# Kernel optimization log

Measured on AMD Instinct MI355X. Metric: run time of the kernel, lower is better.

## Reference

```python
import jax, jax.numpy as jnp
import numpy as np

B = 2_000_000
L = 64
STEPS = 10
LAT_CONST = 5 * 0.03 / 200 + 0.06  # queue*lat/bw + 0.06
GRAD_CONST = 1.0 / 0.06
SEND_CONST = 2.0 / 3.0


def setup_inputs() -> dict:
    key = jax.random.key(0)
    ks = jax.random.split(key, 5)
    x = jax.random.normal(ks[0], (B, 7), dtype=jnp.float32)
    # column 0 is the loop counter i; program assumes it starts at 0 -> 10 iterations
    x = x.at[:, 0].set(0.0)
    W1 = jax.random.normal(ks[1], (3, L), dtype=jnp.float32) * 0.1
    b1 = jnp.zeros((L,), dtype=jnp.float32)
    W2 = jax.random.normal(ks[2], (L, L), dtype=jnp.float32) * 0.1
    b2 = jnp.zeros((L,), dtype=jnp.float32)
    W3 = jax.random.normal(ks[3], (L, 1), dtype=jnp.float32) * 0.1
    b3 = jnp.zeros((1,), dtype=jnp.float32)
    return {"x": x, "W1": W1, "b1": b1, "W2": W2, "b2": b2, "W3": W3, "b3": b3}


def _mlp(feat, W1, b1, W2, b2, W3, b3):
    h = jax.nn.relu(feat @ W1 + b1)
    h = jax.nn.relu(h @ W2 + b2)
    return jax.nn.sigmoid(h @ W3 + b3)[:, 0]


def reference(x, W1, b1, W2, b2, W3, b3):
    def step(state, _):
        x2 = state[:, 2]
        x6 = state[:, 6]
        # IfElse on column 6 vs comparison_bar=0.0:
        #   body  (x6 <= 0): x2 * (x6 + 1)          (assign_upper_sender_ratio)
        #   else  (x6 >  0): x2 * ((1 - x6) / 1)    (assign_down_sender_ratio, sub_l = left-sub)
        x2 = jnp.where(x6 <= 0.0, x2 * (x6 + 1.0), x2 * (1.0 - x6))
        x4 = x2 + LAT_CONST            # latency_ratio
        x5 = x2 * SEND_CONST           # sending_ratio
        x3 = x4 * GRAD_CONST           # latency_gradient
        feat = jnp.stack([x3, x4, x5], axis=1)  # [B,3]
        a = _mlp(feat, W1, b1, W2, b2, W3, b3)  # new action -> column 2
        new_state = state.at[:, 0].add(1.0)
        new_state = new_state.at[:, 2].set(a)
        new_state = new_state.at[:, 3].set(x3)
        new_state = new_state.at[:, 4].set(x4)
        new_state = new_state.at[:, 5].set(x5)
        return new_state, None

    final, _ = jax.lax.scan(step, x, None, length=STEPS)
    return final
```

## Files before the change

kernel.cpp:

```cpp
#include <hip/hip_runtime.h>
#include <math.h>

#define LAT_CONST  ((float)(5.0 * 0.03 / 200.0 + 0.06))
#define GRAD_CONST ((float)(1.0 / 0.06))
#define SEND_CONST ((float)(2.0 / 3.0))

#define NW   2048
#define LOW_ (-24.f)
#define HIW_ (24.f)
#define HW_  ((HIW_ - LOW_) / (float)NW)
#define IHW_ ((float)NW / (HIW_ - LOW_))
#define CW_  (-LOW_ * IHW_)
#define N2   2048
#define LO2  (-6.25f)
#define HI2  (1.25f)
#define H2   ((HI2 - LO2) / (float)N2)
#define IH2  ((float)N2 / (HI2 - LO2))
#define C2   (-LO2 * IH2)

#define GSZ   2080
#define GPCK  2064

typedef unsigned int u32;

__device__ __forceinline__ u32 bfpack(float a, float b) {
    u32 ua = __float_as_uint(a), ub = __float_as_uint(b);
    ua = (ua + 0x7fffu + ((ua >> 16) & 1u)) >> 16;
    ub = (ub + 0x7fffu + ((ub >> 16) & 1u)) & 0xffff0000u;
    return (ua & 0xffffu) | ub;
}

__device__ __forceinline__ float lerp_pk(u32 u, float fr) {
    float e0 = __uint_as_float(u << 16);
    float e1 = __uint_as_float(u & 0xffff0000u);
    return fmaf(e1 - e0, fr, e0);
}

__global__ __launch_bounds__(512)
void build_table_kernel(const float* __restrict__ W1, const float* __restrict__ b1,
                        const float* __restrict__ W2, const float* __restrict__ b2,
                        const float* __restrict__ W3, const float* __restrict__ b3,
                        float* __restrict__ g1, float* __restrict__ g2)
{
    __shared__ float pl[8][64];

    const int lane = threadIdx.x & 63;
    const int w    = threadIdx.x >> 6;
    const int i    = blockIdx.x * 64 + lane;

    float t;
    if (i < GSZ) t = LOW_ + (float)i * HW_;
    else         t = LO2 + (float)(i - GSZ) * H2;

    float x4 = t + LAT_CONST;
    float x5 = t * SEND_CONST;
    float x3 = x4 * GRAD_CONST;

    float h1v[64];
#pragma unroll
    for (int j = 0; j < 64; ++j) {
        float acc = b1[j];
        acc = fmaf(x3, W1[j],       acc);
        acc = fmaf(x4, W1[64 + j],  acc);
        acc = fmaf(x5, W1[128 + j], acc);
        h1v[j] = fmaxf(acc, 0.f);
    }

    const int j0 = w * 8;
    float acc[8];
#pragma unroll
    for (int u = 0; u < 8; ++u) acc[u] = b2[j0 + u];
#pragma unroll
    for (int k = 0; k < 64; ++k) {
        const float* __restrict__ w2r = W2 + k * 64 + j0;
#pragma unroll
        for (int u = 0; u < 8; ++u)
            acc[u] = fmaf(h1v[k], w2r[u], acc[u]);
    }
    float partial = 0.f;
#pragma unroll
    for (int u = 0; u < 8; ++u)
        partial = fmaf(fmaxf(acc[u], 0.f), W3[j0 + u], partial);

    pl[w][lane] = partial;
    __syncthreads();

    if (w == 0) {
        float logit = b3[0] + (((pl[0][lane] + pl[1][lane]) + (pl[2][lane] + pl[3][lane]))
                             + ((pl[4][lane] + pl[5][lane]) + (pl[6][lane] + pl[7][lane])));
        float g = 1.f / (1.f + expf(-logit));
        if (i < GSZ) g1[i] = g;
        else         g2[i - GSZ] = g;
    }
}

__global__ __launch_bounds__(256)
void pack_table_kernel(const float* __restrict__ g1, const float* __restrict__ g2,
                       u32* __restrict__ g1p, u32* __restrict__ g2p)
{
    int i = blockIdx.x * blockDim.x + threadIdx.x;
    if (i < GPCK) {
        g1p[i] = bfpack(g1[i], g1[i + 1]);
        g2p[i] = bfpack(g2[i], g2[i + 1]);
    }
}

#define CHUNK 256
#define BLOCK 256
#define MAXBLK 1792

typedef __attribute__((address_space(3))) u32 lds_u32_t;
typedef __attribute__((address_space(1))) const u32 glb_u32_t;

__device__ __forceinline__ void gload16(const void* g, void* l) {
    __builtin_amdgcn_global_load_lds((glb_u32_t*)g, (lds_u32_t*)l, 16, 0, 0);
}
__device__ __forceinline__ void gload4(const void* g, void* l) {
    __builtin_amdgcn_global_load_lds((glb_u32_t*)g, (lds_u32_t*)l, 4, 0, 0);
}

__global__ __launch_bounds__(BLOCK)
void rows_kernel(const float* __restrict__ x, const u32* __restrict__ g1p,
                 const u32* __restrict__ g2p, float* __restrict__ out,
                 int B, int nChunks, int grid)
{
    __shared__ u32 tn[GPCK];
    __shared__ __align__(16) float buf[2][CHUNK * 7];

    const int tid = threadIdx.x;
    const long long b = blockIdx.x;
    const int cb = (int)(b * (long long)nChunks / grid);
    const int ce = (int)((b + 1) * (long long)nChunks / grid);

    {
        int rows0 = min(CHUNK, B - cb * CHUNK);
        int nfl0  = rows0 * 7;
        int nf40  = nfl0 >> 2;
        const float* src = x + (size_t)cb * CHUNK * 7;
        for (int i = tid; i < nf40; i += BLOCK)
            gload16((const float4*)src + i, &buf[0][i * 4]);
        for (int i = (nf40 << 2) + tid; i < nfl0; i += BLOCK)
            gload4(src + i, &buf[0][i]);
    }
    for (int i = tid; i < GPCK / 4; i += BLOCK)
        ((uint4*)tn)[i] = ((const uint4*)g2p)[i];
    __syncthreads();

    int cur = 0;
    for (int c = cb; c < ce; ++c) {
        if (c + 1 < ce) {
            int rowsN = min(CHUNK, B - (c + 1) * CHUNK);
            int nflN  = rowsN * 7;
            int nf4N  = nflN >> 2;
            const float* src = x + (size_t)(c + 1) * CHUNK * 7;
            for (int i = tid; i < nf4N; i += BLOCK)
                gload16((const float4*)src + i, &buf[cur ^ 1][i * 4]);
            for (int i = (nf4N << 2) + tid; i < nflN; i += BLOCK)
                gload4(src + i, &buf[cur ^ 1][i]);
        }

        int rows = min(CHUNK, B - c * CHUNK);
        float* bfr = buf[cur];
        for (int r = tid; r < rows; r += BLOCK) {
            float* row = bfr + r * 7;
            float x0 = row[0], x2 = row[2], x6 = row[6];
            float f = (x6 <= 0.f) ? (x6 + 1.f) : (1.f - x6);
            {
                float p = fmaf(x2, f * IHW_, CW_);
                p = fminf(fmaxf(p, 0.f), (float)NW);
                int idx = (int)p; float fr = p - (float)idx;
                x2 = lerp_pk(g1p[idx], fr);
            }
            float af2 = f * IH2;
#pragma unroll
            for (int s = 0; s < 8; ++s) {
                float p = fmaf(x2, af2, C2);
                p = fminf(fmaxf(p, 0.f), (float)N2);
                int idx = (int)p; float fr = p - (float)idx;
                u32 u = (s & 1) ? g2p[idx] : tn[idx];
                x2 = lerp_pk(u, fr);
            }
            float t = x2 * f;
            float p = fmaf(t, IH2, C2);
            p = fminf(fmaxf(p, 0.f), (float)N2);
            int idx = (int)p; float fr = p - (float)idx;
            float x2f = lerp_pk(tn[idx], fr);
            float x4 = t + LAT_CONST;
            row[0] = x0 + 10.f;
            row[2] = x2f;
            row[3] = x4 * GRAD_CONST;
            row[4] = x4;
            row[5] = t * SEND_CONST;
        }
        __syncthreads();

        {
            int nfl = rows * 7;
            int nf4 = nfl >> 2;
            float* dst = out + (size_t)c * CHUNK * 7;
            const float4* s4 = (const float4*)bfr;
            for (int i = tid; i < nf4; i += BLOCK) ((float4*)dst)[i] = s4[i];
            for (int i = (nf4 << 2) + tid; i < nfl; i += BLOCK) dst[i] = bfr[i];
        }
        __syncthreads();
        cur ^= 1;
    }
}

static inline size_t align16h(size_t v) { return (v + 15) & ~(size_t)15; }

extern "C" void kernel_launch(void* const* d_in, const int* in_sizes, int n_in,
                              void* d_out, int out_size, void* d_ws, size_t ws_size,
                              hipStream_t stream)
{
    const float* x  = (const float*)d_in[0];
    const float* W1 = (const float*)d_in[1];
    const float* b1 = (const float*)d_in[2];
    const float* W2 = (const float*)d_in[3];
    const float* b2 = (const float*)d_in[4];
    const float* W3 = (const float*)d_in[5];
    const float* b3 = (const float*)d_in[6];
    float* out = (float*)d_out;

    int B = in_sizes[0] / 7;

    char* ws = (char*)d_ws;
    float* g1  = (float*)ws;
    float* g2  = (float*)(ws + align16h((size_t)GSZ * 4));
    u32*   g1p = (u32*)  (ws + 2 * align16h((size_t)GSZ * 4));
    u32*   g2p = (u32*)  (ws + 3 * align16h((size_t)GSZ * 4));

    int nChunks = (B + CHUNK - 1) / CHUNK;
    int grid    = (nChunks < MAXBLK) ? nChunks : MAXBLK;

    hipLaunchKernelGGL(build_table_kernel, dim3((2 * GSZ) / 64), dim3(512), 0, stream,
                       W1, b1, W2, b2, W3, b3, g1, g2);
    hipLaunchKernelGGL(pack_table_kernel, dim3((GPCK + 255) / 256), dim3(256), 0, stream,
                       g1, g2, g1p, g2p);
    hipLaunchKernelGGL(rows_kernel, dim3(grid), dim3(BLOCK), 0, stream,
                       x, g1p, g2p, out, B, nChunks, grid);
}
```

Before: 39.11 us.

## Replace iterated table lookups with Chebyshev polynomial evaluation of the MLP

Fits a 28-term Chebyshev series to the scalar MLP response on the inner range, sampling 64 Chebyshev nodes in the table-build kernel and computing coefficients in the pack kernel. The eight inner per-row steps now evaluate this series with Clenshaw recurrence from register-held coefficients instead of dependent LDS/global table gathers. This removes serial memory-latency chains at the cost of roughly 27 FMAs per step and a different approximation error profile.

```diff
diff --git a/kernel.cpp b/kernel.cpp
--- a/kernel.cpp
+++ b/kernel.cpp
@@ -17,9 +17,14 @@
 #define H2   ((HI2 - LO2) / (float)N2)
 #define IH2  ((float)N2 / (HI2 - LO2))
 #define C2   (-LO2 * IH2)
+#define MID2 (-2.5f)
+#define HALF2 (3.75f)
+#define IHALF2 (1.f / 3.75f)
 
 #define GSZ   2080
 #define GPCK  2064
+#define MCH   64
+#define NCOEF 28
 
 typedef unsigned int u32;
 
@@ -40,7 +45,8 @@
 void build_table_kernel(const float* __restrict__ W1, const float* __restrict__ b1,
                         const float* __restrict__ W2, const float* __restrict__ b2,
                         const float* __restrict__ W3, const float* __restrict__ b3,
-                        float* __restrict__ g1, float* __restrict__ g2)
+                        float* __restrict__ g1, float* __restrict__ g2,
+                        float* __restrict__ fch)
 {
     __shared__ float pl[8][64];
 
@@ -49,8 +55,13 @@
     const int i    = blockIdx.x * 64 + lane;
 
     float t;
-    if (i < GSZ) t = LOW_ + (float)i * HW_;
-    else         t = LO2 + (float)(i - GSZ) * H2;
+    if (i < GSZ)          t = LOW_ + (float)i * HW_;
+    else if (i < 2 * GSZ) t = LO2 + (float)(i - GSZ) * H2;
+    else {
+        int j = i - 2 * GSZ;
+        float th = ((float)j + 0.5f) * ((float)M_PI / (float)MCH);
+        t = MID2 + HALF2 * cosf(th);
+    }
 
     float x4 = t + LAT_CONST;
     float x5 = t * SEND_CONST;
@@ -89,20 +100,33 @@
         float logit = b3[0] + (((pl[0][lane] + pl[1][lane]) + (pl[2][lane] + pl[3][lane]))
                              + ((pl[4][lane] + pl[5][lane]) + (pl[6][lane] + pl[7][lane])));
         float g = 1.f / (1.f + expf(-logit));
-        if (i < GSZ) g1[i] = g;
-        else         g2[i - GSZ] = g;
+        if (i < GSZ)          g1[i] = g;
+        else if (i < 2 * GSZ) g2[i - GSZ] = g;
+        else                  fch[i - 2 * GSZ] = g;
     }
 }
 
 __global__ __launch_bounds__(256)
-void pack_table_kernel(const float* __restrict__ g1, const float* __restrict__ g2,
-                       u32* __restrict__ g1p, u32* __restrict__ g2p)
+void fit_pack_kernel(const float* __restrict__ g1, const float* __restrict__ g2,
+                     const float* __restrict__ fch,
+                     u32* __restrict__ g1p, u32* __restrict__ g2p,
+                     float* __restrict__ cb)
 {
     int i = blockIdx.x * blockDim.x + threadIdx.x;
     if (i < GPCK) {
         g1p[i] = bfpack(g1[i], g1[i + 1]);
         g2p[i] = bfpack(g2[i], g2[i + 1]);
     }
+    if (blockIdx.x == 0 && threadIdx.x < NCOEF) {
+        int k = threadIdx.x;
+        float s = 0.f;
+        for (int j = 0; j < MCH; ++j) {
+            float th = ((float)j + 0.5f) * ((float)M_PI / (float)MCH);
+            s = fmaf(fch[j], cosf((float)k * th), s);
+        }
+        float c = s * (2.f / (float)MCH);
+        cb[k] = (k == 0) ? 0.5f * c : c;
+    }
 }
 
 #define CHUNK 256
@@ -121,22 +145,26 @@
 
 __global__ __launch_bounds__(BLOCK)
 void rows_kernel(const float* __restrict__ x, const u32* __restrict__ g1p,
-                 const u32* __restrict__ g2p, float* __restrict__ out,
-                 int B, int nChunks, int grid)
+                 const u32* __restrict__ g2p, const float* __restrict__ cb,
+                 float* __restrict__ out, int B, int nChunks, int grid)
 {
     __shared__ u32 tn[GPCK];
     __shared__ __align__(16) float buf[2][CHUNK * 7];
 
     const int tid = threadIdx.x;
     const long long b = blockIdx.x;
-    const int cb = (int)(b * (long long)nChunks / grid);
-    const int ce = (int)((b + 1) * (long long)nChunks / grid);
+    const int cb_ = (int)(b * (long long)nChunks / grid);
+    const int ce  = (int)((b + 1) * (long long)nChunks / grid);
+
+    float c[NCOEF];
+#pragma unroll
+    for (int k = 0; k < NCOEF; ++k) c[k] = cb[k];
 
     {
-        int rows0 = min(CHUNK, B - cb * CHUNK);
+        int rows0 = min(CHUNK, B - cb_ * CHUNK);
         int nfl0  = rows0 * 7;
         int nf40  = nfl0 >> 2;
-        const float* src = x + (size_t)cb * CHUNK * 7;
+        const float* src = x + (size_t)cb_ * CHUNK * 7;
         for (int i = tid; i < nf40; i += BLOCK)
             gload16((const float4*)src + i, &buf[0][i * 4]);
         for (int i = (nf40 << 2) + tid; i < nfl0; i += BLOCK)
@@ -147,19 +175,19 @@
     __syncthreads();
 
     int cur = 0;
-    for (int c = cb; c < ce; ++c) {
-        if (c + 1 < ce) {
-            int rowsN = min(CHUNK, B - (c + 1) * CHUNK);
+    for (int cc = cb_; cc < ce; ++cc) {
+        if (cc + 1 < ce) {
+            int rowsN = min(CHUNK, B - (cc + 1) * CHUNK);
             int nflN  = rowsN * 7;
             int nf4N  = nflN >> 2;
-            const float* src = x + (size_t)(c + 1) * CHUNK * 7;
+            const float* src = x + (size_t)(cc + 1) * CHUNK * 7;
             for (int i = tid; i < nf4N; i += BLOCK)
                 gload16((const float4*)src + i, &buf[cur ^ 1][i * 4]);
             for (int i = (nf4N << 2) + tid; i < nflN; i += BLOCK)
                 gload4(src + i, &buf[cur ^ 1][i]);
         }
 
-        int rows = min(CHUNK, B - c * CHUNK);
+        int rows = min(CHUNK, B - cc * CHUNK);
         float* bfr = buf[cur];
         for (int r = tid; r < rows; r += BLOCK) {
             float* row = bfr + r * 7;
@@ -171,14 +199,19 @@
                 int idx = (int)p; float fr = p - (float)idx;
                 x2 = lerp_pk(g1p[idx], fr);
             }
-            float af2 = f * IH2;
 #pragma unroll
             for (int s = 0; s < 8; ++s) {
-                float p = fmaf(x2, af2, C2);
-                p = fminf(fmaxf(p, 0.f), (float)N2);
-                int idx = (int)p; float fr = p - (float)idx;
-                u32 u = (s & 1) ? g2p[idx] : tn[idx];
-                x2 = lerp_pk(u, fr);
+                float t = x2 * f;
+                t = fminf(fmaxf(t, LO2), HI2);
+                float u  = (t - MID2) * IHALF2;
+                float u2 = u + u;
+                float b1_ = 0.f, b2_ = 0.f;
+#pragma unroll
+                for (int k = NCOEF - 1; k >= 1; --k) {
+                    float bn = fmaf(u2, b1_, c[k] - b2_);
+                    b2_ = b1_; b1_ = bn;
+                }
+                x2 = fmaf(u, b1_, c[0] - b2_);
             }
             float t = x2 * f;
             float p = fmaf(t, IH2, C2);
@@ -197,7 +230,7 @@
         {
             int nfl = rows * 7;
             int nf4 = nfl >> 2;
-            float* dst = out + (size_t)c * CHUNK * 7;
+            float* dst = out + (size_t)cc * CHUNK * 7;
             const float4* s4 = (const float4*)bfr;
             for (int i = tid; i < nf4; i += BLOCK) ((float4*)dst)[i] = s4[i];
             for (int i = (nf4 << 2) + tid; i < nfl; i += BLOCK) dst[i] = bfr[i];
@@ -225,18 +258,21 @@
     int B = in_sizes[0] / 7;
 
     char* ws = (char*)d_ws;
+    size_t seg = align16h((size_t)GSZ * 4);
     float* g1  = (float*)ws;
-    float* g2  = (float*)(ws + align16h((size_t)GSZ * 4));
-    u32*   g1p = (u32*)  (ws + 2 * align16h((size_t)GSZ * 4));
-    u32*   g2p = (u32*)  (ws + 3 * align16h((size_t)GSZ * 4));
+    float* g2  = (float*)(ws + seg);
+    u32*   g1p = (u32*)  (ws + 2 * seg);
+    u32*   g2p = (u32*)  (ws + 3 * seg);
+    float* fch = (float*)(ws + 4 * seg);
+    float* cb  = (float*)(ws + 4 * seg + align16h(MCH * 4));
 
     int nChunks = (B + CHUNK - 1) / CHUNK;
     int grid    = (nChunks < MAXBLK) ? nChunks : MAXBLK;
 
-    hipLaunchKernelGGL(build_table_kernel, dim3((2 * GSZ) / 64), dim3(512), 0, stream,
-                       W1, b1, W2, b2, W3, b3, g1, g2);
-    hipLaunchKernelGGL(pack_table_kernel, dim3((GPCK + 255) / 256), dim3(256), 0, stream,
-                       g1, g2, g1p, g2p);
+    hipLaunchKernelGGL(build_table_kernel, dim3((2 * GSZ + MCH) / 64), dim3(512), 0, stream,
+                       W1, b1, W2, b2, W3, b3, g1, g2, fch);
+    hipLaunchKernelGGL(fit_pack_kernel, dim3((GPCK + 255) / 256), dim3(256), 0, stream,
+                       g1, g2, fch, g1p, g2p, cb);
     hipLaunchKernelGGL(rows_kernel, dim3(grid), dim3(BLOCK), 0, stream,
-                       x, g1p, g2p, out, B, nChunks, grid);
-}
+                       x, g1p, g2p, cb, out, B, nChunks, grid);
+}
```

Result: slower. 53.52 us (+36.8%).
